# Kernel optimization log

Measured on AMD Instinct MI355X. Metric: run time of the kernel, lower is better.

Reference implementation:

```python
import jax, jax.numpy as jnp
import numpy as np

S, B, F, H, L, T = 256, 64, 256, 768, 3, 32  # seq_len, batch, features, hidden, layers, target_len


def setup_inputs() -> dict:
    key = jax.random.key(0)
    ks = jax.random.split(key, 16)
    s = 1.0 / np.sqrt(H)  # PyTorch LSTM/Linear uniform init bound
    u = lambda k, shape: jax.random.uniform(k, shape, jnp.float32, -s, s)
    return {
        "x": jax.random.normal(ks[0], (S, B, F), jnp.float32),
        # encoder layer 0: input_size -> hidden_size
        "e_Wih0": u(ks[1], (4 * H, F)), "e_Whh0": u(ks[2], (4 * H, H)),
        "e_bih0": u(ks[3], (4 * H,)), "e_bhh0": u(ks[4], (4 * H,)),
        # encoder layers 1..L-1 (stacked): hidden -> hidden
        "e_Wih": u(ks[5], (L - 1, 4 * H, H)), "e_Whh": u(ks[6], (L - 1, 4 * H, H)),
        "e_bih": u(ks[7], (L - 1, 4 * H)), "e_bhh": u(ks[8], (L - 1, 4 * H)),
        # decoder layers (stacked): hidden -> hidden
        "d_Wih": u(ks[9], (L, 4 * H, H)), "d_Whh": u(ks[10], (L, 4 * H, H)),
        "d_bih": u(ks[11], (L, 4 * H)), "d_bhh": u(ks[12], (L, 4 * H)),
        # output head: hidden -> input_size
        "lin_W": u(ks[13], (F, H)), "lin_b": u(ks[14], (F,)),
        "target_len": T,
    }


def _cell(gates, c_prev):
    # PyTorch gate order: input, forget, cell(g), output
    i, f, g, o = jnp.split(gates, 4, axis=-1)
    c = jax.nn.sigmoid(f) * c_prev + jax.nn.sigmoid(i) * jnp.tanh(g)
    h = jax.nn.sigmoid(o) * jnp.tanh(c)
    return h, c


def reference(x, e_Wih0, e_Whh0, e_bih0, e_bhh0, e_Wih, e_Whh, e_bih, e_bhh,
              d_Wih, d_Whh, d_bih, d_bhh, lin_W, lin_b, target_len):
    Bb = x.shape[1]
    Hh = e_Whh0.shape[1]
    dt = x.dtype

    # --- encoder layer 0: full-sequence LSTM from zero state ---
    b0 = e_bih0 + e_bhh0
    def enc_step(carry, x_t):
        h, c = carry
        h, c = _cell(x_t @ e_Wih0.T + h @ e_Whh0.T + b0, c)
        return (h, c), None
    z = jnp.zeros((Bb, Hh), dt)
    (h, _), _ = jax.lax.scan(enc_step, (z, z), x)

    # --- encoder layers 1..L-1: each sees previous layer's final hidden as a
    # seq_len=1 input with fresh zero (h0, c0) -> W_hh term vanishes ---
    enc = [h]
    xin = h
    for l in range(e_Wih.shape[0]):
        hl, _ = _cell(xin @ e_Wih[l].T + (e_bih[l] + e_bhh[l]), 0.0)
        enc.append(hl)
        xin = hl
    encoder_hidden = jnp.stack(enc)  # (L, B, H)

    # --- decoder: recursive. Call-site bug passes zeros as initial hidden_list.
    # Each step, each layer i independently runs a 1-step LSTM on its own previous
    # hidden with fresh zero state (W_hh unused, cell not carried). Only the last
    # layer's hidden feeds the Linear head. ---
    d_b = (d_bih + d_bhh)[:, None, :]  # (L, 1, 4H)
    def dec_step(hs, _):
        gates = jnp.einsum('lbh,lgh->lbg', hs, d_Wih) + d_b
        hn, _ = _cell(gates, 0.0)
        out_t = hn[-1] @ lin_W.T + lin_b  # (B, F)
        return hn, out_t
    h0 = jnp.zeros((d_Wih.shape[0], Bb, Hh), dt)
    _, outputs = jax.lax.scan(dec_step, h0, None, length=target_len)  # (T, B, F)

    return outputs, encoder_hidden
```

## Files before the change

kernel.cpp:

```cpp
#include <hip/hip_runtime.h>
#include <hip/hip_bf16.h>


constexpr int NB = 64;
constexpr int NH = 768;
constexpr int NF = 256;
constexpr int NS = 256;
constexpr int NT = 32;
constexpr int ENC_BLOCKS = 96;
constexpr int DEC_BLOCKS = 48;

typedef short bf16x8 __attribute__((ext_vector_type(8)));
typedef float f32x4 __attribute__((ext_vector_type(4)));

__device__ __forceinline__ float sigm(float x) { return 1.f / (1.f + expf(-x)); }

__device__ __forceinline__ int4 ld_i4_cohere(const int4* p) {
    int4 v;
    asm volatile("global_load_dwordx4 %0, %1, off sc0 sc1" : "=v"(v) : "v"(p));
    return v;
}
__device__ __forceinline__ void st_i1_cohere(int* p, int v) {
    asm volatile("global_store_dword %0, %1, off sc0 sc1" :: "v"(p), "v"(v) : "memory");
}
__device__ __forceinline__ void vm_drain() {
    asm volatile("s_waitcnt vmcnt(0)" ::: "memory");
}

__device__ __forceinline__ void arrive(int* slots, int phase) {
    if (threadIdx.x == 0)
        __hip_atomic_store(slots + (int)blockIdx.x * 16, phase,
                           __ATOMIC_RELAXED, __HIP_MEMORY_SCOPE_AGENT);
}
__device__ __forceinline__ void wait_all(int* slots, int phase, int nb) {
    if (threadIdx.x < 64)
        for (int s = threadIdx.x; s < nb; s += 64)
            while (__hip_atomic_load(slots + s * 16, __ATOMIC_RELAXED,
                                     __HIP_MEMORY_SCOPE_AGENT) < phase)
                __builtin_amdgcn_s_sleep(1);
    __syncthreads();
}

__global__ __launch_bounds__(256) void cvt_f32_bf16(
    const float* __restrict__ s, __hip_bfloat16* __restrict__ d, int n)
{
    const int i = (blockIdx.x * 256 + threadIdx.x) * 4;
    if (i >= n) return;
    const float4 v = *(const float4*)(s + i);
    d[i]     = __float2bfloat16(v.x);
    d[i + 1] = __float2bfloat16(v.y);
    d[i + 2] = __float2bfloat16(v.z);
    d[i + 3] = __float2bfloat16(v.w);
}

__global__ __launch_bounds__(256, 1) void enc_persist(
    const __hip_bfloat16* __restrict__ xb,
    const __hip_bfloat16* __restrict__ Wx,
    const __hip_bfloat16* __restrict__ Wh,
    const float* __restrict__ bih, const float* __restrict__ bhh,
    int* __restrict__ h0buf,
    int* __restrict__ h1buf,
    float* __restrict__ enc0,
    int* slots)
{
    const int bu = blockIdx.x % (NH / 16);
    const int bm = blockIdx.x / (NH / 16);
    const int u0 = bu * 16;
    const int tid = threadIdx.x;
    const int g = tid >> 6;
    const int lane = tid & 63;
    const int r = lane & 15;
    const int q = lane >> 4;
    const int row0 = bm * 32 + r;
    const int row1 = row0 + 16;

    const size_t wrow = (size_t)(g * NH + u0 + r);
    bf16x8 wx[8], wh[24];
    #pragma unroll
    for (int c = 0; c < 8; ++c)
        wx[c] = *(const bf16x8*)(Wx + wrow * NF + c * 32 + q * 8);
    #pragma unroll
    for (int c = 0; c < 24; ++c)
        wh[c] = *(const bf16x8*)(Wh + wrow * NH + c * 32 + q * 8);

    __shared__ int   hst[32 * 388];
    __shared__ float gbuf[4][32][17];
    __shared__ float lbias[64];
    if (tid < 64)
        lbias[tid] = bih[(tid >> 4) * NH + u0 + (tid & 15)]
                   + bhh[(tid >> 4) * NH + u0 + (tid & 15)];
    __syncthreads();

    float cst[2] = {0.f, 0.f};

    for (int t = 0; t < NS; ++t) {
        const int* hcur = (t & 1) ? h1buf : h0buf;
        int* hnext      = (t & 1) ? h0buf : h1buf;
        const __hip_bfloat16* xt = xb + (size_t)t * NB * NF;

        f32x4 acc0 = {0.f, 0.f, 0.f, 0.f};
        f32x4 acc1 = {0.f, 0.f, 0.f, 0.f};
        #pragma unroll
        for (int c = 0; c < 8; ++c) {
            const bf16x8 a0 = *(const bf16x8*)(xt + (size_t)row0 * NF + c * 32 + q * 8);
            const bf16x8 a1 = *(const bf16x8*)(xt + (size_t)row1 * NF + c * 32 + q * 8);
            acc0 = __builtin_amdgcn_mfma_f32_16x16x32_bf16(a0, wx[c], acc0, 0, 0, 0);
            acc1 = __builtin_amdgcn_mfma_f32_16x16x32_bf16(a1, wx[c], acc1, 0, 0, 0);
        }

        if (t > 0) wait_all(slots, t, ENC_BLOCKS);

        {
            const int4* src = (const int4*)hcur + bm * 3072;
            int4 v[12];
            #pragma unroll
            for (int i = 0; i < 12; ++i) v[i] = ld_i4_cohere(src + i * 256 + tid);
            vm_drain();
            #pragma unroll
            for (int i = 0; i < 12; ++i) {
                const int k = i * 256 + tid;
                const int rw = k / 96, cl = k % 96;
                *(int4*)(hst + rw * 388 + cl * 4) = v[i];
            }
        }
        __syncthreads();

        #pragma unroll
        for (int c = 0; c < 24; ++c) {
            const bf16x8 a0 = *(const bf16x8*)((const short*)hst + r * 776 + c * 32 + q * 8);
            const bf16x8 a1 = *(const bf16x8*)((const short*)hst + (r + 16) * 776 + c * 32 + q * 8);
            acc0 = __builtin_amdgcn_mfma_f32_16x16x32_bf16(a0, wh[c], acc0, 0, 0, 0);
            acc1 = __builtin_amdgcn_mfma_f32_16x16x32_bf16(a1, wh[c], acc1, 0, 0, 0);
        }

        #pragma unroll
        for (int i = 0; i < 4; ++i) {
            gbuf[g][q * 4 + i][r]      = acc0[i];
            gbuf[g][16 + q * 4 + i][r] = acc1[i];
        }
        __syncthreads();

        {
            const int rowl = tid >> 3, pair = tid & 7;
            const int ua = pair * 2;
            float h2[2];
            #pragma unroll
            for (int e = 0; e < 2; ++e) {
                const int ul = ua + e;
                const float pi = gbuf[0][rowl][ul] + lbias[ul];
                const float pf = gbuf[1][rowl][ul] + lbias[16 + ul];
                const float pg = gbuf[2][rowl][ul] + lbias[32 + ul];
                const float po = gbuf[3][rowl][ul] + lbias[48 + ul];
                const float cn = sigm(pf) * cst[e] + sigm(pi) * tanhf(pg);
                h2[e] = sigm(po) * tanhf(cn);
                cst[e] = cn;
            }
            const int b = bm * 32 + rowl;
            if (t == NS - 1) {
                enc0[(size_t)b * NH + u0 + ua]     = h2[0];
                enc0[(size_t)b * NH + u0 + ua + 1] = h2[1];
                __hip_bfloat16* hf = (__hip_bfloat16*)hnext;
                hf[(size_t)b * NH + u0 + ua]     = __float2bfloat16(h2[0]);
                hf[(size_t)b * NH + u0 + ua + 1] = __float2bfloat16(h2[1]);
            } else {
                union { __hip_bfloat16 b16; unsigned short s; } c0, c1;
                c0.b16 = __float2bfloat16(h2[0]);
                c1.b16 = __float2bfloat16(h2[1]);
                const int pv = (int)c0.s | ((int)c1.s << 16);
                st_i1_cohere(hnext + (size_t)b * 384 + (u0 >> 1) + pair, pv);
            }
        }
        if (t < NS - 1) {
            vm_drain();
            __syncthreads();
            arrive(slots, t + 1);
        }
    }
}

template<int KX, int KH>
__global__ __launch_bounds__(256) void lstm_step(
    const __hip_bfloat16* __restrict__ xin,
    const __hip_bfloat16* __restrict__ hin,
    const __hip_bfloat16* __restrict__ Wx,
    const __hip_bfloat16* __restrict__ Wh,
    const float* __restrict__ bih, const float* __restrict__ bhh,
    const float* __restrict__ c_in,
    __hip_bfloat16* __restrict__ h_bf,
    float* __restrict__ h_f32,
    float* __restrict__ c_out)
{
    constexpr int K = KX + KH;
    constexpr int NCH = K / 32;
    const int bu = blockIdx.x % (NH / 16);
    const int bm = blockIdx.x / (NH / 16);
    const int u0 = bu * 16;
    const int tid = threadIdx.x;
    const int g = tid >> 6;
    const int lane = tid & 63;
    const int r = lane & 15;
    const int q = lane >> 4;

    f32x4 acc0 = {0.f, 0.f, 0.f, 0.f};
    f32x4 acc1 = {0.f, 0.f, 0.f, 0.f};
    const int row0 = bm * 32 + r;
    const int row1 = row0 + 16;
    const long wr = (long)(g * NH + u0 + r);

    #pragma unroll
    for (int c = 0; c < NCH; ++c) {
        const int k0 = c * 32;
        bf16x8 a0, a1, bfrag;
        if (k0 < KX) {
            const int kk = k0 + q * 8;
            a0 = *(const bf16x8*)(xin + (long)row0 * KX + kk);
            a1 = *(const bf16x8*)(xin + (long)row1 * KX + kk);
            bfrag = *(const bf16x8*)(Wx + wr * KX + kk);
        } else {
            const int kk = (k0 - KX) + q * 8;
            a0 = *(const bf16x8*)(hin + (long)row0 * KH + kk);
            a1 = *(const bf16x8*)(hin + (long)row1 * KH + kk);
            bfrag = *(const bf16x8*)(Wh + wr * KH + kk);
        }
        acc0 = __builtin_amdgcn_mfma_f32_16x16x32_bf16(a0, bfrag, acc0, 0, 0, 0);
        acc1 = __builtin_amdgcn_mfma_f32_16x16x32_bf16(a1, bfrag, acc1, 0, 0, 0);
    }

    __shared__ float gbuf[4][32][17];
    #pragma unroll
    for (int i = 0; i < 4; ++i) {
        gbuf[g][q * 4 + i][r]      = acc0[i];
        gbuf[g][16 + q * 4 + i][r] = acc1[i];
    }
    __syncthreads();

    #pragma unroll
    for (int i = 0; i < 2; ++i) {
        const int idx = tid + i * 256;
        const int bl = idx >> 4;
        const int u  = idx & 15;
        const int gu = u0 + u;
        const int b  = bm * 32 + bl;
        const float pi = gbuf[0][bl][u] + bih[gu]          + bhh[gu];
        const float pf = gbuf[1][bl][u] + bih[NH + gu]     + bhh[NH + gu];
        const float pg = gbuf[2][bl][u] + bih[2 * NH + gu] + bhh[2 * NH + gu];
        const float po = gbuf[3][bl][u] + bih[3 * NH + gu] + bhh[3 * NH + gu];
        const float cp = c_in ? c_in[(long)b * NH + gu] : 0.f;
        const float cn = sigm(pf) * cp + sigm(pi) * tanhf(pg);
        const float hn = sigm(po) * tanhf(cn);
        if (c_out) c_out[(long)b * NH + gu] = cn;
        if (h_f32) h_f32[(long)b * NH + gu] = hn;
        h_bf[(long)b * NH + gu] = __float2bfloat16(hn);
    }
}

__global__ __launch_bounds__(256) void dec_persist(
    const float* __restrict__ W,
    const float* __restrict__ bih, const float* __restrict__ bhh,
    float* __restrict__ hd0, float* __restrict__ hd1,
    float* __restrict__ hall, int* slots)
{
    __shared__ float hstD[768];
    const int tid = threadIdx.x;
    const int ul = tid >> 4;
    const int j  = tid & 15;
    const int u  = blockIdx.x * 16 + ul;
    const float* Wi = W + (size_t)u * NH;
    const float* Wg = W + (size_t)(2 * NH + u) * NH;
    const float* Wo = W + (size_t)(3 * NH + u) * NH;
    const float bi = bih[u]          + bhh[u];
    const float bg = bih[2 * NH + u] + bhh[2 * NH + u];
    const float bo = bih[3 * NH + u] + bhh[3 * NH + u];

    for (int t = 0; t < NT; ++t) {
        const float* hin = (t & 1) ? hd1 : hd0;
        float* hout      = (t & 1) ? hd0 : hd1;
        if (t > 0) wait_all(slots, t, DEC_BLOCKS);
        if (tid < 192) {
            int4 v = ld_i4_cohere((const int4*)hin + tid);
            vm_drain();
            ((int4*)hstD)[tid] = v;
        }
        __syncthreads();
        float ai = 0.f, ag = 0.f, ao = 0.f;
        for (int k = j; k < NH; k += 16) {
            const float hv = hstD[k];
            ai += hv * Wi[k];
            ag += hv * Wg[k];
            ao += hv * Wo[k];
        }
        #pragma unroll
        for (int off = 8; off > 0; off >>= 1) {
            ai += __shfl_xor(ai, off, 16);
            ag += __shfl_xor(ag, off, 16);
            ao += __shfl_xor(ao, off, 16);
        }
        if (j == 0) {
            const float cn = sigm(ai + bi) * tanhf(ag + bg);
            const float hn = sigm(ao + bo) * tanhf(cn);
            hall[(size_t)t * NH + u] = hn;
            if (t < NT - 1)
                st_i1_cohere((int*)(hout + u), __float_as_int(hn));
        }
        if (t < NT - 1) {
            vm_drain();
            __syncthreads();
            arrive(slots, t + 1);
        }
    }
}

__global__ __launch_bounds__(256) void head_kernel(
    const float* __restrict__ hall,
    const float* __restrict__ lw,
    const float* __restrict__ lb,
    float* __restrict__ out)
{
    const int t = blockIdx.x;
    const int f = threadIdx.x;
    const float* h = hall + (size_t)t * NH;
    const float4* wrow = (const float4*)(lw + (size_t)f * NH);
    float acc = 0.f;
    for (int k4 = 0; k4 < NH / 4; ++k4) {
        const float4 w = wrow[k4];
        acc += h[k4 * 4]     * w.x;
        acc += h[k4 * 4 + 1] * w.y;
        acc += h[k4 * 4 + 2] * w.z;
        acc += h[k4 * 4 + 3] * w.w;
    }
    acc += lb[f];
    float* o = out + (size_t)t * NB * NF + f;
    for (int b = 0; b < NB; ++b) o[(size_t)b * NF] = acc;
}

extern "C" void kernel_launch(void* const* d_in, const int* in_sizes, int n_in,
                              void* d_out, int out_size, void* d_ws, size_t ws_size,
                              hipStream_t stream) {
    (void)in_sizes; (void)n_in; (void)out_size; (void)ws_size;
    const float* x     = (const float*)d_in[0];
    const float* eWih0 = (const float*)d_in[1];
    const float* eWhh0 = (const float*)d_in[2];
    const float* ebih0 = (const float*)d_in[3];
    const float* ebhh0 = (const float*)d_in[4];
    const float* eWih  = (const float*)d_in[5];
    const float* ebih  = (const float*)d_in[7];
    const float* ebhh  = (const float*)d_in[8];
    const float* dWih  = (const float*)d_in[9];
    const float* dbih  = (const float*)d_in[11];
    const float* dbhh  = (const float*)d_in[12];
    const float* linW  = (const float*)d_in[13];
    const float* linb  = (const float*)d_in[14];
    float* out = (float*)d_out;

    char* ws = (char*)d_ws;
    __hip_bfloat16* xb   = (__hip_bfloat16*)(ws);
    __hip_bfloat16* W0x  = (__hip_bfloat16*)(ws +  8388608);
    __hip_bfloat16* W0h  = (__hip_bfloat16*)(ws +  9961472);
    __hip_bfloat16* eW12 = (__hip_bfloat16*)(ws + 14680064);
    int* hbi0 = (int*)(ws + 24117248);
    int* hbi1 = (int*)(ws + 24215552);
    float* hd0  = (float*)(ws + 24313856);
    float* hd1  = (float*)(ws + 24316928);
    float* hall = (float*)(ws + 24320000);
    int* bar    = (int*)(ws + 24418304);
    int* enc_slots = bar;
    int* dec_slots = bar + 1536;

    (void)hipMemsetAsync(hbi0, 0, (size_t)NB * NH * 2, stream);
    (void)hipMemsetAsync(hd0, 0, (size_t)NH * 4, stream);
    (void)hipMemsetAsync(bar, 0, 16384, stream);

    cvt_f32_bf16<<<(NS * NB * NF) / 1024, 256, 0, stream>>>(x, xb, NS * NB * NF);
    cvt_f32_bf16<<<(4 * NH * NF) / 1024, 256, 0, stream>>>(eWih0, W0x, 4 * NH * NF);
    cvt_f32_bf16<<<(4 * NH * NH) / 1024, 256, 0, stream>>>(eWhh0, W0h, 4 * NH * NH);
    cvt_f32_bf16<<<(2 * 4 * NH * NH) / 1024, 256, 0, stream>>>(eWih, eW12, 2 * 4 * NH * NH);

    float* enc = out + (size_t)NT * NB * NF;

    enc_persist<<<ENC_BLOCKS, 256, 0, stream>>>(
        xb, W0x, W0h, ebih0, ebhh0, hbi0, hbi1, enc, enc_slots);

    __hip_bfloat16* hb0 = (__hip_bfloat16*)hbi0;
    __hip_bfloat16* hb1 = (__hip_bfloat16*)hbi1;
    lstm_step<NH, 0><<<96, 256, 0, stream>>>(
        hb0, nullptr, eW12, nullptr, ebih, ebhh,
        nullptr, hb1, enc + NB * NH, nullptr);
    lstm_step<NH, 0><<<96, 256, 0, stream>>>(
        hb1, nullptr, eW12 + (size_t)4 * NH * NH, nullptr,
        ebih + 4 * NH, ebhh + 4 * NH,
        nullptr, hb0, enc + 2 * (size_t)NB * NH, nullptr);

    const float* W2 = dWih + (size_t)2 * 4 * NH * NH;
    dec_persist<<<DEC_BLOCKS, 256, 0, stream>>>(
        W2, dbih + 2 * 4 * NH, dbhh + 2 * 4 * NH, hd0, hd1, hall, dec_slots);

    head_kernel<<<NT, NF, 0, stream>>>(hall, linW, linb, out);
}
```

Baseline: 1.866 ms.

## Split encoder barrier into per-batch-half groups and fuse conversion kernels

The encoder grid barrier now waits only on the 48 blocks that share the same batch half (bm), because each half reads only its own rows of the hidden state. Barrier arrive and poll now use coherent sc0/sc1 global store and load instead of relaxed agent atomics, with one thread polling each slot. The four fp32-to-bf16 conversion launches are merged into one kernel that indexes into the contiguous workspace. The narrower barrier relies on each batch half's h buffer being written only by blocks of that same half.

```diff
diff --git a/kernel.cpp b/kernel.cpp
--- a/kernel.cpp
+++ b/kernel.cpp
@@ -8,6 +8,7 @@
 constexpr int NS = 256;
 constexpr int NT = 32;
 constexpr int ENC_BLOCKS = 96;
+constexpr int ENC_GROUP  = 48;
 constexpr int DEC_BLOCKS = 48;
 
 typedef short bf16x8 __attribute__((ext_vector_type(8)));
@@ -20,6 +21,12 @@
     asm volatile("global_load_dwordx4 %0, %1, off sc0 sc1" : "=v"(v) : "v"(p));
     return v;
 }
+__device__ __forceinline__ int ld_i1_cohere_sync(const int* p) {
+    int v;
+    asm volatile("global_load_dword %0, %1, off sc0 sc1\n\ts_waitcnt vmcnt(0)"
+                 : "=v"(v) : "v"(p) : "memory");
+    return v;
+}
 __device__ __forceinline__ void st_i1_cohere(int* p, int v) {
     asm volatile("global_store_dword %0, %1, off sc0 sc1" :: "v"(p), "v"(v) : "memory");
 }
@@ -27,26 +34,31 @@
     asm volatile("s_waitcnt vmcnt(0)" ::: "memory");
 }
 
-__device__ __forceinline__ void arrive(int* slots, int phase) {
-    if (threadIdx.x == 0)
-        __hip_atomic_store(slots + (int)blockIdx.x * 16, phase,
-                           __ATOMIC_RELAXED, __HIP_MEMORY_SCOPE_AGENT);
+__device__ __forceinline__ void arrive(int* slots, int idx, int phase) {
+    if (threadIdx.x == 0) st_i1_cohere(slots + idx * 16, phase);
 }
 __device__ __forceinline__ void wait_all(int* slots, int phase, int nb) {
-    if (threadIdx.x < 64)
-        for (int s = threadIdx.x; s < nb; s += 64)
-            while (__hip_atomic_load(slots + s * 16, __ATOMIC_RELAXED,
-                                     __HIP_MEMORY_SCOPE_AGENT) < phase)
-                __builtin_amdgcn_s_sleep(1);
+    if (threadIdx.x < nb) {
+        const int* p = slots + threadIdx.x * 16;
+        while (ld_i1_cohere_sync(p) < phase) __builtin_amdgcn_s_sleep(1);
+    }
     __syncthreads();
 }
 
-__global__ __launch_bounds__(256) void cvt_f32_bf16(
-    const float* __restrict__ s, __hip_bfloat16* __restrict__ d, int n)
+__global__ __launch_bounds__(256) void cvt_all(
+    const float* __restrict__ s0,
+    const float* __restrict__ s1,
+    const float* __restrict__ s2,
+    const float* __restrict__ s3,
+    __hip_bfloat16* __restrict__ d)
 {
     const int i = (blockIdx.x * 256 + threadIdx.x) * 4;
-    if (i >= n) return;
-    const float4 v = *(const float4*)(s + i);
+    const float* s; int off;
+    if (i < 4194304)      { s = s0; off = 0; }
+    else if (i < 4980736) { s = s1; off = 4194304; }
+    else if (i < 7340032) { s = s2; off = 4980736; }
+    else                  { s = s3; off = 7340032; }
+    const float4 v = *(const float4*)(s + (i - off));
     d[i]     = __float2bfloat16(v.x);
     d[i + 1] = __float2bfloat16(v.y);
     d[i + 2] = __float2bfloat16(v.z);
@@ -65,6 +77,7 @@
 {
     const int bu = blockIdx.x % (NH / 16);
     const int bm = blockIdx.x / (NH / 16);
+    int* gslots = slots + bm * ENC_GROUP * 16;
     const int u0 = bu * 16;
     const int tid = threadIdx.x;
     const int g = tid >> 6;
@@ -108,7 +121,7 @@
             acc1 = __builtin_amdgcn_mfma_f32_16x16x32_bf16(a1, wx[c], acc1, 0, 0, 0);
         }
 
-        if (t > 0) wait_all(slots, t, ENC_BLOCKS);
+        if (t > 0) wait_all(gslots, t, ENC_GROUP);
 
         {
             const int4* src = (const int4*)hcur + bm * 3072;
@@ -173,7 +186,7 @@
         if (t < NS - 1) {
             vm_drain();
             __syncthreads();
-            arrive(slots, t + 1);
+            arrive(gslots, bu, t + 1);
         }
     }
 }
@@ -305,7 +318,7 @@
         if (t < NT - 1) {
             vm_drain();
             __syncthreads();
-            arrive(slots, t + 1);
+            arrive(slots, blockIdx.x, t + 1);
         }
     }
 }
@@ -364,16 +377,14 @@
     float* hall = (float*)(ws + 24320000);
     int* bar    = (int*)(ws + 24418304);
     int* enc_slots = bar;
-    int* dec_slots = bar + 1536;
+    int* dec_slots = bar + 2048;
 
     (void)hipMemsetAsync(hbi0, 0, (size_t)NB * NH * 2, stream);
     (void)hipMemsetAsync(hd0, 0, (size_t)NH * 4, stream);
     (void)hipMemsetAsync(bar, 0, 16384, stream);
 
-    cvt_f32_bf16<<<(NS * NB * NF) / 1024, 256, 0, stream>>>(x, xb, NS * NB * NF);
-    cvt_f32_bf16<<<(4 * NH * NF) / 1024, 256, 0, stream>>>(eWih0, W0x, 4 * NH * NF);
-    cvt_f32_bf16<<<(4 * NH * NH) / 1024, 256, 0, stream>>>(eWhh0, W0h, 4 * NH * NH);
-    cvt_f32_bf16<<<(2 * 4 * NH * NH) / 1024, 256, 0, stream>>>(eWih, eW12, 2 * 4 * NH * NH);
+    cvt_all<<<12058624 / 1024, 256, 0, stream>>>(x, eWih0, eWhh0, eWih,
+                                                 (__hip_bfloat16*)ws);
 
     float* enc = out + (size_t)NT * NB * NF;
 
```

Measured after the change: 1.792 ms. 3.9% less time.
